# Optimization experiments

Hardware: AMD Instinct MI355X
Metric: run time of the kernel (lower is better)

The kernel has to match this reference:

```python
import jax, jax.numpy as jnp
import numpy as np

LN_EPS = 1e-5
DIM = 128
HEADS = 6
DIM_HEAD = 32
INNER = HEADS * DIM_HEAD          # 192
FF_INNER = int(DIM * 4 * 2 / 3)   # 341 (GEGLU inner dim)
LOCAL_WINDOW = 200
CACHE = 3
COMPRESS = 2
TW = LOCAL_WINDOW + CACHE         # 203
B = 2
T = 12800                         # 32 chunks of 400


def layer_norm(x, w, b):
    m = x.mean(-1, keepdims=True)
    v = ((x - m) ** 2).mean(-1, keepdims=True)
    return (x - m) / jnp.sqrt(v + LN_EPS) * w + b


def apply_rotary(q, k):
    # q, k: (b, h, n, d); standard half-rotation rotary over absolute positions
    d = q.shape[-1]
    n = q.shape[2]
    inv_freq = 1.0 / (10000.0 ** (jnp.arange(0, d, 2, dtype=jnp.float32) / d))
    freqs = jnp.arange(n, dtype=jnp.float32)[:, None] * inv_freq  # (n, d/2)
    emb = jnp.concatenate([freqs, freqs], axis=-1)                # (n, d)
    cos = jnp.cos(emb).astype(q.dtype)
    sin = jnp.sin(emb).astype(q.dtype)

    def rot_half(x):
        x1, x2 = jnp.split(x, 2, axis=-1)
        return jnp.concatenate([-x2, x1], axis=-1)

    rope = lambda x: x * cos + rot_half(x) * sin
    return rope(q), rope(k)


def local_attention(q, k, v, w):
    # causal local attention, look_backward=1 window, look_forward=0 (lucidrains LocalAttention)
    b, h, n, d = q.shape
    nw = n // w
    q, k = apply_rotary(q, k)
    qw = q.reshape(b, h, nw, w, d)

    def look_around(x):
        xw = x.reshape(b, h, nw, w, d)
        prev = jnp.pad(xw[:, :, :-1], ((0, 0), (0, 0), (1, 0), (0, 0), (0, 0)))
        return jnp.concatenate([prev, xw], axis=3)  # (b,h,nw,2w,d)

    kw = look_around(k)
    vw = look_around(v)

    t = jnp.arange(n).reshape(nw, w)
    tk_prev = jnp.pad(t[:-1], ((1, 0), (0, 0)), constant_values=-1)
    tk = jnp.concatenate([tk_prev, t], axis=1)  # (nw, 2w); -1 marks padding
    mask = (t[:, :, None] >= tk[:, None, :]) & (tk[:, None, :] >= 0)  # (nw, w, 2w)

    sim = jnp.einsum('bhwid,bhwjd->bhwij', qw, kw) * (d ** -0.5)
    neg = jnp.finfo(sim.dtype).min
    sim = jnp.where(mask[None, None], sim, neg)
    attn = jax.nn.softmax(sim, axis=-1)
    out = jnp.einsum('bhwij,bhwjd->bhwid', attn, vw)
    return out.reshape(b, h, n, d)


def local_mha(x, ln_w, ln_b, wqkv, wo, window):
    h = layer_norm(x, ln_w, ln_b)
    qkv = h @ wqkv                       # (b, n, 3*INNER)
    q, k, v = jnp.split(qkv, 3, axis=-1)

    def split_heads(t):
        bb, n, _ = t.shape
        return t.reshape(bb, n, HEADS, DIM_HEAD).transpose(0, 2, 1, 3)

    out = local_attention(split_heads(q), split_heads(k), split_heads(v), window)
    bb, hh, n, d = out.shape
    out = out.transpose(0, 2, 1, 3).reshape(bb, n, hh * d)
    return out @ wo


def feed_forward(x, ln_w, ln_b, w1, w2):
    h = layer_norm(x, ln_w, ln_b) @ w1   # (b, n, 2*FF_INNER)
    a, gate = jnp.split(h, 2, axis=-1)
    return (a * jax.nn.gelu(gate, approximate=False)) @ w2


def local_trans(x, ln1_w, ln1_b, wqkv, wo, ln2_w, ln2_b, w1, w2, window):
    n_layers = ln1_w.shape[0]
    for i in range(n_layers):
        x = x + local_mha(x, ln1_w[i], ln1_b[i], wqkv[i], wo[i], window)
        x = x + feed_forward(x, ln2_w[i], ln2_b[i], w1[i], w2[i])
    return x


def setup_inputs() -> dict:
    key = jax.random.key(0)
    ks = jax.random.split(key, 16)
    std = 0.02
    rn = lambda k, shape: jax.random.normal(k, shape, dtype=jnp.float32) * std
    inp = {
        'x': jax.random.normal(ks[0], (B, DIM, T), dtype=jnp.float32),
        'cache_token': jax.random.normal(ks[1], (1, CACHE * COMPRESS, DIM), dtype=jnp.float32),
    }
    ki = 2
    for g in ('dt', 'lt'):
        inp[g + '_ln1_w'] = jnp.ones((2, DIM), jnp.float32)
        inp[g + '_ln1_b'] = jnp.zeros((2, DIM), jnp.float32)
        inp[g + '_wqkv'] = rn(ks[ki], (2, DIM, 3 * INNER)); ki += 1
        inp[g + '_wo'] = rn(ks[ki], (2, INNER, DIM)); ki += 1
        inp[g + '_ln2_w'] = jnp.ones((2, DIM), jnp.float32)
        inp[g + '_ln2_b'] = jnp.zeros((2, DIM), jnp.float32)
        inp[g + '_w1'] = rn(ks[ki], (2, DIM, 2 * FF_INNER)); ki += 1
        inp[g + '_w2'] = rn(ks[ki], (2, FF_INNER, DIM)); ki += 1
    inp['conv_w'] = rn(ks[ki], (DIM, DIM, COMPRESS)); ki += 1
    inp['conv_b'] = jnp.zeros((DIM,), jnp.float32)
    return inp


def reference(x, cache_token,
              dt_ln1_w, dt_ln1_b, dt_wqkv, dt_wo, dt_ln2_w, dt_ln2_b, dt_w1, dt_w2,
              lt_ln1_w, lt_ln1_b, lt_wqkv, lt_wo, lt_ln2_w, lt_ln2_b, lt_w1, lt_w2,
              conv_w, conv_b):
    feat = x.transpose(0, 2, 1)                     # (B, T, C)
    b, t, c = feat.shape
    chunk = LOCAL_WINDOW * COMPRESS                 # 400
    nchunks = t // chunk
    feat = feat.reshape(b, nchunks, chunk, c)
    ct = jnp.broadcast_to(cache_token[:, None], (b, nchunks, CACHE * COMPRESS, c))
    feat = jnp.concatenate([ct, feat], axis=2)      # interleave cache tokens per chunk
    feat = feat.reshape(b, nchunks * (chunk + CACHE * COMPRESS), c)

    # DownTrans: 2-layer local transformer (window 406) + strided conv compress
    feat = local_trans(feat, dt_ln1_w, dt_ln1_b, dt_wqkv, dt_wo,
                       dt_ln2_w, dt_ln2_b, dt_w1, dt_w2, TW * COMPRESS)
    y = jax.lax.conv_general_dilated(
        feat.transpose(0, 2, 1), conv_w, (COMPRESS,), 'VALID',
        dimension_numbers=('NCH', 'OIH', 'NCH')) + conv_b[None, :, None]
    feat = y.transpose(0, 2, 1)                     # (B, n/2, C)

    # remaining depth-2 local transformer (window 203)
    feat = local_trans(feat, lt_ln1_w, lt_ln1_b, lt_wqkv, lt_wo,
                       lt_ln2_w, lt_ln2_b, lt_w1, lt_w2, TW)
    return feat
```

## Files before the change

kernel.cpp:

```cpp
#include <hip/hip_runtime.h>
#include <cstdint>
#include <cstddef>

#define DIM    128
#define HEADS  6
#define INNER  192
#define QKV3   576
#define FFI    341
#define FF2    682
#define GGP    352
#define BATCH  2
#define T_IN   12800
#define N1     12992
#define N2     6496
#define ROWS1  (BATCH * N1)
#define ROWS2  (BATCH * N2)
#define W_DT   406
#define W_LT   203

typedef unsigned short ushortT;
typedef unsigned int u32;
typedef __bf16 bf16x8 __attribute__((ext_vector_type(8)));
typedef float f32x4 __attribute__((ext_vector_type(4)));

__device__ __forceinline__ f32x4 mfma16(bf16x8 a, bf16x8 b, f32x4 c) {
  return __builtin_amdgcn_mfma_f32_16x16x32_bf16(a, b, c, 0, 0, 0);
}
__device__ __forceinline__ ushortT f2bf(float x) {
  union { __bf16 b; ushortT u; } c; c.b = (__bf16)x; return c.u;
}
__device__ __forceinline__ void async_copy16(const ushortT* g, ushortT* l) {
  __builtin_amdgcn_global_load_lds(
      (const __attribute__((address_space(1))) unsigned int*)g,
      (__attribute__((address_space(3))) unsigned int*)l, 16, 0, 0);
}

static constexpr size_t OF_FEAT = 0;
static constexpr size_t OF_H    = OF_FEAT + (size_t)ROWS1 * DIM;
static constexpr size_t OF_QKH  = OF_H + (size_t)ROWS1 * DIM / 2;
static constexpr size_t SZ_QKH  = ((size_t)(ROWS1 + 128) * 384) / 2;
static constexpr size_t OF_AO   = OF_QKH + SZ_QKH;
static constexpr size_t OF_VT   = OF_AO + (size_t)ROWS1 * INNER / 2;
static constexpr size_t SZ_VT   = ((size_t)384 * (N1 + 128)) / 2;
static constexpr size_t OF_GG   = OF_VT + SZ_VT;
static constexpr size_t OF_F2   = OF_GG + (size_t)ROWS1 * GGP / 2;
static constexpr size_t OF_WT   = OF_F2 + (size_t)ROWS2 * DIM;
static constexpr size_t WT_QKV = 0;
static constexpr size_t WT_WO  = 81920;
static constexpr size_t WT_W1  = 106496;
static constexpr size_t WT_W2  = 204800;
static constexpr size_t WT_SET = 249856;
static constexpr size_t OF_CW  = OF_WT + (4 * WT_SET) / 2 + 64;

__global__ void build_feat_kernel(const float* __restrict__ x,
                                  const float* __restrict__ cache,
                                  float* __restrict__ feat) {
  int idx = blockIdx.x * 256 + threadIdx.x;
  if (idx >= ROWS1 * DIM) return;
  int d = idx & 127;
  int row = idx >> 7;
  int b = row / N1;
  int i = row - b * N1;
  int c = i / 406;
  int j = i - c * 406;
  float v;
  if (j < 6) v = cache[j * DIM + d];
  else       v = x[((size_t)b * DIM + d) * T_IN + (c * 400 + j - 6)];
  feat[idx] = v;
}

__global__ __launch_bounds__(256) void ln_kernel(const float* __restrict__ x,
                                                 ushortT* __restrict__ y,
                                                 const float* __restrict__ w,
                                                 const float* __restrict__ bb,
                                                 int rows) {
  int row = blockIdx.x * 4 + (threadIdx.x >> 6);
  if (row >= rows) return;
  int lane = threadIdx.x & 63;
  const float* xr = x + (size_t)row * DIM;
  float2 v = *(const float2*)(xr + lane * 2);
  float s = v.x + v.y;
#pragma unroll
  for (int off = 32; off; off >>= 1) s += __shfl_xor(s, off);
  float mean = s * (1.0f / 128.0f);
  float dx = v.x - mean, dy = v.y - mean;
  float q = dx * dx + dy * dy;
#pragma unroll
  for (int off = 32; off; off >>= 1) q += __shfl_xor(q, off);
  float rstd = rsqrtf(q * (1.0f / 128.0f) + 1e-5f);
  float2 wv = *(const float2*)(w + lane * 2);
  float2 bv = *(const float2*)(bb + lane * 2);
  u32 packed = (u32)f2bf(dx * rstd * wv.x + bv.x) |
               ((u32)f2bf(dy * rstd * wv.y + bv.y) << 16);
  *(u32*)(y + (size_t)row * DIM + lane * 2) = packed;
}

__global__ __launch_bounds__(256) void gemm_nln(
    const ushortT* __restrict__ A, int lda,
    const ushortT* __restrict__ Wt, int ldw,
    const float* __restrict__ C, float* __restrict__ Co,
    int M, int Kpad, int addC,
    const float* __restrict__ lnw, const float* __restrict__ lnb,
    ushortT* __restrict__ hout) {
  __shared__ ushortT As[64 * 32];
  __shared__ ushortT Bs[128 * 32];
  __shared__ float lnS[64][4];
  const int tid = threadIdx.x;
  const int wid = tid >> 6, lane = tid & 63;
  const int ck = lane & 15, quad = lane >> 4;
  const int bm = blockIdx.y * 64;
  const int wr = (wid >> 1) * 32, wc = (wid & 1) * 64;
  const int half = wid & 1;
  f32x4 acc[2][4];
#pragma unroll
  for (int t = 0; t < 2; t++)
#pragma unroll
    for (int u = 0; u < 4; u++) acc[t][u] = (f32x4){0.f, 0.f, 0.f, 0.f};

  for (int k0 = 0; k0 < Kpad; k0 += 32) {
    __syncthreads();
    {
      int idx = wid * 64 + lane;
      int row = idx >> 2, seg = (idx & 3) << 3;
      async_copy16(A + (size_t)(bm + row) * lda + k0 + seg, As + (size_t)(wid * 64) * 8);
    }
#pragma unroll
    for (int c2 = 0; c2 < 2; c2++) {
      int idx = c2 * 256 + wid * 64 + lane;
      int row = idx >> 2, seg = (idx & 3) << 3;
      async_copy16(Wt + (size_t)row * ldw + k0 + seg, Bs + (size_t)(c2 * 256 + wid * 64) * 8);
    }
    __syncthreads();
    bf16x8 af[2], bfr[4];
#pragma unroll
    for (int t = 0; t < 2; t++)
      af[t] = *(const bf16x8*)&As[(wr + t * 16 + ck) * 32 + quad * 8];
#pragma unroll
    for (int u = 0; u < 4; u++)
      bfr[u] = *(const bf16x8*)&Bs[(wc + u * 16 + ck) * 32 + quad * 8];
#pragma unroll
    for (int t = 0; t < 2; t++)
#pragma unroll
      for (int u = 0; u < 4; u++)
        acc[t][u] = mfma16(af[t], bfr[u], acc[t][u]);
  }

  float res[2][4][4];
#pragma unroll
  for (int t = 0; t < 2; t++) {
#pragma unroll
    for (int r = 0; r < 4; r++) {
      int row = bm + wr + t * 16 + quad * 4 + r;
      const float* crow = C + (size_t)row * DIM;
      float* orow = Co + (size_t)row * DIM;
#pragma unroll
      for (int u = 0; u < 4; u++) {
        int col = wc + u * 16 + ck;
        float v = acc[t][u][r];
        if (addC) v += crow[col];
        res[t][r][u] = v;
        orow[col] = v;
      }
    }
  }

  if (hout) {
#pragma unroll
    for (int t = 0; t < 2; t++) {
#pragma unroll
      for (int r = 0; r < 4; r++) {
        float s1 = ((res[t][r][0] + res[t][r][1]) + (res[t][r][2] + res[t][r][3]));
        float s2 = ((res[t][r][0] * res[t][r][0] + res[t][r][1] * res[t][r][1]) +
                    (res[t][r][2] * res[t][r][2] + res[t][r][3] * res[t][r][3]));
        s1 += __shfl_xor(s1, 1); s2 += __shfl_xor(s2, 1);
        s1 += __shfl_xor(s1, 2); s2 += __shfl_xor(s2, 2);
        s1 += __shfl_xor(s1, 4); s2 += __shfl_xor(s2, 4);
        s1 += __shfl_xor(s1, 8); s2 += __shfl_xor(s2, 8);
        if (ck == 0) {
          int rowIn = wr + t * 16 + quad * 4 + r;
          lnS[rowIn][half * 2]     = s1;
          lnS[rowIn][half * 2 + 1] = s2;
        }
      }
    }
    __syncthreads();
    float lw[4], lb[4];
#pragma unroll
    for (int u = 0; u < 4; u++) {
      lw[u] = lnw[wc + u * 16 + ck];
      lb[u] = lnb[wc + u * 16 + ck];
    }
#pragma unroll
    for (int t = 0; t < 2; t++) {
#pragma unroll
      for (int r = 0; r < 4; r++) {
        int rowIn = wr + t * 16 + quad * 4 + r;
        float S1 = lnS[rowIn][0] + lnS[rowIn][2];
        float S2 = lnS[rowIn][1] + lnS[rowIn][3];
        float mean = S1 * (1.0f / 128.0f);
        float var = S2 * (1.0f / 128.0f) - mean * mean;
        float rstd = rsqrtf(var + 1e-5f);
        ushortT* hrow = hout + (size_t)(bm + rowIn) * DIM;
#pragma unroll
        for (int u = 0; u < 4; u++) {
          int col = wc + u * 16 + ck;
          hrow[col] = f2bf((res[t][r][u] - mean) * rstd * lw[u] + lb[u]);
        }
      }
    }
  }
}

__global__ __launch_bounds__(256) void gemm_qkv(
    const ushortT* __restrict__ A,
    const ushortT* __restrict__ Wt,
    ushortT* __restrict__ qkh,
    ushortT* __restrict__ vt,
    int M, int nseq, int nseqP) {
  __shared__ ushortT As[128 * 32];
  __shared__ ushortT Bs[128 * 32];
  const int tid = threadIdx.x;
  const int wid = tid >> 6, lane = tid & 63;
  const int ck = lane & 15, quad = lane >> 4;
  const int bm = blockIdx.y * 128, bn = blockIdx.x * 128;
  const int wr = (wid >> 1) * 64, wc = (wid & 1) * 64;
  f32x4 acc[4][4];
#pragma unroll
  for (int t = 0; t < 4; t++)
#pragma unroll
    for (int u = 0; u < 4; u++) acc[t][u] = (f32x4){0.f, 0.f, 0.f, 0.f};

  for (int k0 = 0; k0 < 128; k0 += 32) {
    __syncthreads();
#pragma unroll
    for (int c2 = 0; c2 < 2; c2++) {
      int idx = c2 * 256 + wid * 64 + lane;
      int row = idx >> 2, seg = (idx & 3) << 3;
      int ar = bm + row; if (ar > M - 1) ar = M - 1;
      async_copy16(A + (size_t)ar * 128 + k0 + seg, As + (size_t)(c2 * 256 + wid * 64) * 8);
      async_copy16(Wt + (size_t)(bn + row) * 128 + k0 + seg, Bs + (size_t)(c2 * 256 + wid * 64) * 8);
    }
    __syncthreads();
    bf16x8 af[4], bfr[4];
#pragma unroll
    for (int t = 0; t < 4; t++)
      af[t] = *(const bf16x8*)&As[(wr + t * 16 + ck) * 32 + quad * 8];
#pragma unroll
    for (int u = 0; u < 4; u++)
      bfr[u] = *(const bf16x8*)&Bs[(wc + u * 16 + ck) * 32 + quad * 8];
#pragma unroll
    for (int t = 0; t < 4; t++)
#pragma unroll
      for (int u = 0; u < 4; u++)
        acc[t][u] = mfma16(af[t], bfr[u], acc[t][u]);
  }

  const int s = bn + wc;
  if (s >= QKV3) return;

  if (s < 384) {
    const bool isQ = s < 192;
    const float SCq = 0.17677669529663687f * 1.4426950408889634f;
    const float invf = 1.0f / powf(10000.0f, (float)ck * (1.0f / 16.0f));
#pragma unroll
    for (int t = 0; t < 4; t++) {
#pragma unroll
      for (int r = 0; r < 4; r++) {
        int row = bm + wr + t * 16 + quad * 4 + r;
        if (row >= M) continue;
        int pos = (row >= nseq) ? row - nseq : row;
        float sn, cs;
        sincosf((float)pos * invf, &sn, &cs);
        ushortT* orow = qkh + (size_t)row * 384;
#pragma unroll
        for (int u = 0; u < 4; u += 2) {
          float a0 = acc[t][u][r], a1 = acc[t][u + 1][r];
          float o0 = a0 * cs - a1 * sn;
          float o1 = a1 * cs + a0 * sn;
          if (isQ) { o0 *= SCq; o1 *= SCq; }
          int c0 = s + u * 16 + ck;
          orow[c0]      = f2bf(o0);
          orow[c0 + 16] = f2bf(o1);
        }
      }
    }
  } else {
#pragma unroll
    for (int t = 0; t < 4; t++) {
      int rowb = bm + wr + t * 16 + quad * 4;
      if (rowb >= M) continue;
      int bb = (rowb >= nseq) ? 1 : 0;
      int posb = rowb - bb * nseq;
#pragma unroll
      for (int u = 0; u < 4; u++) {
        int cv = s - 384 + u * 16 + ck;
        int hh = cv >> 5, d = cv & 31;
        ushort4 o;
        o.x = f2bf(acc[t][u][0]);
        o.y = f2bf(acc[t][u][1]);
        o.z = f2bf(acc[t][u][2]);
        o.w = f2bf(acc[t][u][3]);
        *(ushort4*)(vt + ((size_t)((bb * 6 + hh) * 32 + d)) * nseqP + posb) = o;
      }
    }
  }
}

__global__ __launch_bounds__(256) void gemm_w1g(
    const ushortT* __restrict__ A,
    const ushortT* __restrict__ Wt,
    ushortT* __restrict__ gg,
    int M) {
  __shared__ ushortT As[128 * 32];
  __shared__ ushortT Bs[128 * 32];
  const int tid = threadIdx.x;
  const int wid = tid >> 6, lane = tid & 63;
  const int ck = lane & 15, quad = lane >> 4;
  const int bm = blockIdx.y * 128, bn = blockIdx.x * 128;
  const int wr = (wid >> 1) * 64, wc = (wid & 1) * 64;
  f32x4 acc[4][4];
#pragma unroll
  for (int t = 0; t < 4; t++)
#pragma unroll
    for (int u = 0; u < 4; u++) acc[t][u] = (f32x4){0.f, 0.f, 0.f, 0.f};

  for (int k0 = 0; k0 < 128; k0 += 32) {
    __syncthreads();
#pragma unroll
    for (int c2 = 0; c2 < 2; c2++) {
      int idx = c2 * 256 + wid * 64 + lane;
      int row = idx >> 2, seg = (idx & 3) << 3;
      int ar = bm + row; if (ar > M - 1) ar = M - 1;
      async_copy16(A + (size_t)ar * 128 + k0 + seg, As + (size_t)(c2 * 256 + wid * 64) * 8);
      async_copy16(Wt + (size_t)(bn + row) * 128 + k0 + seg, Bs + (size_t)(c2 * 256 + wid * 64) * 8);
    }
    __syncthreads();
    bf16x8 af[4], bfr[4];
#pragma unroll
    for (int t = 0; t < 4; t++)
      af[t] = *(const bf16x8*)&As[(wr + t * 16 + ck) * 32 + quad * 8];
#pragma unroll
    for (int u = 0; u < 4; u++)
      bfr[u] = *(const bf16x8*)&Bs[(wc + u * 16 + ck) * 32 + quad * 8];
#pragma unroll
    for (int t = 0; t < 4; t++)
#pragma unroll
      for (int u = 0; u < 4; u++)
        acc[t][u] = mfma16(af[t], bfr[u], acc[t][u]);
  }

  const int s = bn + wc;
  if (s >= 704) return;
#pragma unroll
  for (int t = 0; t < 4; t++) {
#pragma unroll
    for (int r = 0; r < 4; r++) {
      int row = bm + wr + t * 16 + quad * 4 + r;
      if (row >= M) continue;
      ushortT* orow = gg + (size_t)row * GGP;
#pragma unroll
      for (int u = 0; u < 4; u += 2) {
        float a  = acc[t][u][r];
        float gt = acc[t][u + 1][r];
        float ge = 0.5f * gt * (1.0f + erff(gt * 0.70710678118654752f));
        int p = ((s + u * 16) >> 5) * 16 + ck;
        orow[p] = f2bf(a * ge);
      }
    }
  }
}

__global__ __launch_bounds__(256) void gemm_f32(
    const float* __restrict__ A, int lda,
    const float* __restrict__ W, int ldw,
    float* __restrict__ C, int ldc,
    int M, int N, int K, int addC, const float* __restrict__ bias) {
  __shared__ float As[16][68];
  __shared__ float Ws[16][68];
  int tid = threadIdx.x;
  int bm = blockIdx.y * 64, bn = blockIdx.x * 64;
  int tx = tid & 15, ty = tid >> 4;
  float acc[4][4] = {{0.f,0.f,0.f,0.f},{0.f,0.f,0.f,0.f},{0.f,0.f,0.f,0.f},{0.f,0.f,0.f,0.f}};
  int arow = tid >> 2;
  int akq = (tid & 3) << 2;
  int wk = tid >> 4;
  int wn = (tid & 15) << 2;
  for (int k0 = 0; k0 < K; k0 += 16) {
    float4 av = *(const float4*)(A + (size_t)(bm + arow) * lda + k0 + akq);
    float4 wv = *(const float4*)(W + (size_t)(k0 + wk) * ldw + bn + wn);
    __syncthreads();
    As[akq + 0][arow] = av.x; As[akq + 1][arow] = av.y;
    As[akq + 2][arow] = av.z; As[akq + 3][arow] = av.w;
    *(float4*)&Ws[wk][wn] = wv;
    __syncthreads();
#pragma unroll
    for (int kk = 0; kk < 16; kk++) {
      float4 a4 = *(const float4*)&As[kk][ty << 2];
      float4 b4 = *(const float4*)&Ws[kk][tx << 2];
      float aa[4] = {a4.x, a4.y, a4.z, a4.w};
      float bv2[4] = {b4.x, b4.y, b4.z, b4.w};
#pragma unroll
      for (int i = 0; i < 4; i++)
#pragma unroll
        for (int j = 0; j < 4; j++)
          acc[i][j] = fmaf(aa[i], bv2[j], acc[i][j]);
    }
  }
#pragma unroll
  for (int i = 0; i < 4; i++) {
    int row = bm + (ty << 2) + i;
    float* crow = C + (size_t)row * ldc;
#pragma unroll
    for (int j = 0; j < 4; j++) {
      int col = bn + (tx << 2) + j;
      float v = acc[i][j];
      if (bias) v += bias[col];
      if (addC) v += crow[col];
      crow[col] = v;
    }
  }
}

__global__ __launch_bounds__(256) void attn_kernel(
    const ushortT* __restrict__ qkh, const ushortT* __restrict__ vt,
    ushortT* __restrict__ out, int nseq, int nseqP, int w, int nw) {
  __shared__ ushortT Ks[128 * 40];
  __shared__ ushortT Vs[32 * 136];
  __shared__ ushortT Ps[4 * 16 * 72];

  const int bx = blockIdx.x;
  const int c = bx % nw;
  const int g = bx / nw;
  const int h = blockIdx.y;
  const int b = blockIdx.z;
  const int tid = threadIdx.x;
  const int wv = tid >> 6;
  const int lane = tid & 63;
  const int ck = lane & 15;
  const int quad = lane >> 4;

  const ushortT* gq = qkh + (size_t)b * nseq * 384;
  const ushortT* gv = vt + ((size_t)(b * 6 + h) * 32) * nseqP;
  const int cw = c * w;
  const int q0 = g * 64;
  const int qt = q0 + wv * 16;
  const bool wave_on = qt < w;

  const int j0 = (c > 0) ? (c - 1) * w : 0;
  const int jend_block = cw + min(q0 + 63, w - 1) + 1;
  const int jend_wave = wave_on ? (cw + min(qt + 15, w - 1) + 1) : 0;

  bf16x8 qf;
  {
    int qrow = cw + min(qt + ck, w - 1);
    qf = *(const bf16x8*)(gq + (size_t)qrow * 384 + h * 32 + quad * 8);
  }

  f32x4 olo = {0.f, 0.f, 0.f, 0.f};
  f32x4 ohi = {0.f, 0.f, 0.f, 0.f};
  float lp[4] = {0.f, 0.f, 0.f, 0.f};
  ushortT* pw = Ps + wv * 16 * 72;

  for (int tb = j0; tb < jend_block; tb += 128) {
    __syncthreads();
    for (int i = tid; i < 512; i += 256) {
      int row = i >> 2, dg = (i & 3) << 3;
      *(float4*)&Ks[row * 40 + dg] =
          *(const float4*)(gq + (size_t)(tb + row) * 384 + 192 + h * 32 + dg);
    }
    for (int i = tid; i < 512; i += 256) {
      int d = i >> 4, kg = (i & 15) << 3;
      *(float4*)&Vs[d * 136 + kg] = *(const float4*)(gv + (size_t)d * nseqP + tb + kg);
    }
    __syncthreads();

    const int glim = min(128, jend_wave - tb);
    for (int g64 = 0; g64 < glim; g64 += 64) {
      int r0 = g64 + 2 * ck;
      bf16x8 kf0 = *(const bf16x8*)&Ks[(r0) * 40 + quad * 8];
      bf16x8 kf1 = *(const bf16x8*)&Ks[(r0 + 1) * 40 + quad * 8];
      bf16x8 kf2 = *(const bf16x8*)&Ks[(r0 + 32) * 40 + quad * 8];
      bf16x8 kf3 = *(const bf16x8*)&Ks[(r0 + 33) * 40 + quad * 8];
      f32x4 z = {0.f, 0.f, 0.f, 0.f};
      f32x4 s0 = mfma16(qf, kf0, z);
      f32x4 s1 = mfma16(qf, kf1, z);
      f32x4 s2 = mfma16(qf, kf2, z);
      f32x4 s3 = mfma16(qf, kf3, z);
      if (tb + g64 + 63 > cw + qt) {
        int key0 = tb + g64 + 2 * ck;
#pragma unroll
        for (int r = 0; r < 4; r++) {
          int qg = cw + qt + quad * 4 + r;
          if (key0 > qg)      s0[r] = -__builtin_inff();
          if (key0 + 1 > qg)  s1[r] = -__builtin_inff();
          if (key0 + 32 > qg) s2[r] = -__builtin_inff();
          if (key0 + 33 > qg) s3[r] = -__builtin_inff();
        }
      }
#pragma unroll
      for (int r = 0; r < 4; r++) {
        float p0 = exp2f(s0[r]);
        float p1 = exp2f(s1[r]);
        float p2 = exp2f(s2[r]);
        float p3 = exp2f(s3[r]);
        lp[r] += (p0 + p1) + (p2 + p3);
        int row72 = (quad * 4 + r) * 72;
        *(u32*)&pw[row72 + 2 * ck]      = (u32)f2bf(p0) | ((u32)f2bf(p1) << 16);
        *(u32*)&pw[row72 + 32 + 2 * ck] = (u32)f2bf(p2) | ((u32)f2bf(p3) << 16);
      }
      bf16x8 pf0 = *(const bf16x8*)&pw[ck * 72 + quad * 8];
      bf16x8 pf1 = *(const bf16x8*)&pw[ck * 72 + 32 + quad * 8];
      bf16x8 vlo0 = *(const bf16x8*)&Vs[ck * 136 + g64 + quad * 8];
      bf16x8 vhi0 = *(const bf16x8*)&Vs[(ck + 16) * 136 + g64 + quad * 8];
      bf16x8 vlo1 = *(const bf16x8*)&Vs[ck * 136 + g64 + 32 + quad * 8];
      bf16x8 vhi1 = *(const bf16x8*)&Vs[(ck + 16) * 136 + g64 + 32 + quad * 8];
      olo = mfma16(pf0, vlo0, olo);
      olo = mfma16(pf1, vlo1, olo);
      ohi = mfma16(pf0, vhi0, ohi);
      ohi = mfma16(pf1, vhi1, ohi);
    }
  }

  if (wave_on) {
#pragma unroll
    for (int r = 0; r < 4; r++) {
      float lr = lp[r];
      lr += __shfl_xor(lr, 1);
      lr += __shfl_xor(lr, 2);
      lr += __shfl_xor(lr, 4);
      lr += __shfl_xor(lr, 8);
      int qi = qt + quad * 4 + r;
      if (qi < w) {
        float inv = 1.0f / lr;
        ushortT* orow = out + ((size_t)b * nseq + cw + qi) * INNER + h * 32;
        orow[ck]      = f2bf(olo[r] * inv);
        orow[ck + 16] = f2bf(ohi[r] * inv);
      }
    }
  }
}

__global__ void wconvert_all_kernel(
    const float* __restrict__ dq, const float* __restrict__ dwo,
    const float* __restrict__ dw1, const float* __restrict__ dw2,
    const float* __restrict__ lq, const float* __restrict__ lwo,
    const float* __restrict__ lw1, const float* __restrict__ lw2,
    const float* __restrict__ convw,
    ushortT* __restrict__ wt, float* __restrict__ cwout) {
  int idx = blockIdx.x * 256 + threadIdx.x;
  const int TOTW = 4 * (int)WT_SET;
  if (idx < TOTW) {
    int s = idx / (int)WT_SET;
    int rem = idx - s * (int)WT_SET;
    int lyr = s & 1;
    const float* Wq = ((s < 2) ? dq : lq) + (size_t)lyr * DIM * QKV3;
    const float* Wo = ((s < 2) ? dwo : lwo) + (size_t)lyr * INNER * DIM;
    const float* W1 = ((s < 2) ? dw1 : lw1) + (size_t)lyr * DIM * FF2;
    const float* W2 = ((s < 2) ? dw2 : lw2) + (size_t)lyr * FFI * DIM;
    float v = 0.f;
    if (rem < (int)WT_WO) {
      int n = rem >> 7, k = rem & 127;
      if (n < QKV3) v = Wq[(size_t)k * QKV3 + n];
    } else if (rem < (int)WT_W1) {
      int r = rem - (int)WT_WO;
      int n = r / INNER, k = r - n * INNER;
      v = Wo[(size_t)k * DIM + n];
    } else if (rem < (int)WT_W2) {
      int r = rem - (int)WT_W1;
      int n = r >> 7, k = r & 127;
      if (n < 704) {
        int blk = n >> 5, wi = n & 31;
        int p = blk * 16 + (wi & 15);
        if (p < FFI) {
          int src = (wi < 16) ? p : FFI + p;
          v = W1[(size_t)k * FF2 + src];
        }
      }
    } else {
      int r = rem - (int)WT_W2;
      int n = r / GGP, k = r - n * GGP;
      if (k < FFI) v = W2[(size_t)k * DIM + n];
    }
    wt[idx] = f2bf(v);
  } else {
    int r = idx - TOTW;
    if (r < 256 * DIM) {
      int kidx = r >> 7, o = r & 127;
      int kk = kidx >> 7, i = kidx & 127;
      cwout[r] = convw[((size_t)o * DIM + i) * 2 + kk];
    }
  }
}

static void run_layer(float* F, float* Fout, ushortT* h, ushortT* qkh, ushortT* vtb,
                      ushortT* attnb, ushortT* ggb, const ushortT* wt,
                      int M, int nseq, int w,
                      const float* ln2w, const float* ln2b,
                      const float* nlnw, const float* nlnb,
                      hipStream_t stream) {
  int nseqP = nseq + 128;
  int gy = (M + 127) / 128;
  int gy64 = M / 64;
  gemm_qkv<<<dim3(5, gy), 256, 0, stream>>>(h, wt + WT_QKV, qkh, vtb, M, nseq, nseqP);
  int nw = nseq / w;
  int qgroups = (w + 63) / 64;
  attn_kernel<<<dim3(nw * qgroups, HEADS, BATCH), 256, 0, stream>>>(qkh, vtb, attnb,
                                                                    nseq, nseqP, w, nw);
  gemm_nln<<<dim3(1, gy64), 256, 0, stream>>>(attnb, INNER, wt + WT_WO, INNER, F, F,
                                              M, INNER, 1, ln2w, ln2b, h);
  gemm_w1g<<<dim3(6, gy), 256, 0, stream>>>(h, wt + WT_W1, ggb, M);
  gemm_nln<<<dim3(1, gy64), 256, 0, stream>>>(ggb, GGP, wt + WT_W2, GGP, F, Fout,
                                              M, GGP, 1, nlnw, nlnb,
                                              nlnw ? h : (ushortT*)nullptr);
}

extern "C" void kernel_launch(void* const* d_in, const int* in_sizes, int n_in,
                              void* d_out, int out_size, void* d_ws, size_t ws_size,
                              hipStream_t stream) {
  const float* x        = (const float*)d_in[0];
  const float* cache    = (const float*)d_in[1];
  const float* dt_ln1_w = (const float*)d_in[2];
  const float* dt_ln1_b = (const float*)d_in[3];
  const float* dt_wqkv  = (const float*)d_in[4];
  const float* dt_wo    = (const float*)d_in[5];
  const float* dt_ln2_w = (const float*)d_in[6];
  const float* dt_ln2_b = (const float*)d_in[7];
  const float* dt_w1    = (const float*)d_in[8];
  const float* dt_w2    = (const float*)d_in[9];
  const float* lt_ln1_w = (const float*)d_in[10];
  const float* lt_ln1_b = (const float*)d_in[11];
  const float* lt_wqkv  = (const float*)d_in[12];
  const float* lt_wo    = (const float*)d_in[13];
  const float* lt_ln2_w = (const float*)d_in[14];
  const float* lt_ln2_b = (const float*)d_in[15];
  const float* lt_w1    = (const float*)d_in[16];
  const float* lt_w2    = (const float*)d_in[17];
  const float* conv_w   = (const float*)d_in[18];
  const float* conv_b   = (const float*)d_in[19];

  float* ws     = (float*)d_ws;
  float* feat   = ws + OF_FEAT;
  ushortT* h    = (ushortT*)(ws + OF_H);
  ushortT* qkh  = (ushortT*)(ws + OF_QKH);
  ushortT* attnb= (ushortT*)(ws + OF_AO);
  ushortT* vtb  = (ushortT*)(ws + OF_VT);
  ushortT* ggb  = (ushortT*)(ws + OF_GG);
  float* feat2  = ws + OF_F2;
  ushortT* wt   = (ushortT*)(ws + OF_WT);
  float* cw     = ws + OF_CW;
  float* outf   = (float*)d_out;

  {
    int total = 4 * (int)WT_SET + 256 * DIM;
    wconvert_all_kernel<<<(total + 255) / 256, 256, 0, stream>>>(
        dt_wqkv, dt_wo, dt_w1, dt_w2, lt_wqkv, lt_wo, lt_w1, lt_w2,
        conv_w, wt, cw);
  }

  build_feat_kernel<<<(ROWS1 * DIM + 255) / 256, 256, 0, stream>>>(x, cache, feat);
  ln_kernel<<<ROWS1 / 4, 256, 0, stream>>>(feat, h, dt_ln1_w, dt_ln1_b, ROWS1);

  run_layer(feat, feat, h, qkh, vtb, attnb, ggb, wt + 0 * WT_SET,
            ROWS1, N1, W_DT,
            dt_ln2_w, dt_ln2_b, dt_ln1_w + DIM, dt_ln1_b + DIM, stream);
  run_layer(feat, feat, h, qkh, vtb, attnb, ggb, wt + 1 * WT_SET,
            ROWS1, N1, W_DT,
            dt_ln2_w + DIM, dt_ln2_b + DIM, nullptr, nullptr, stream);

  gemm_f32<<<dim3(DIM / 64, ROWS2 / 64), 256, 0, stream>>>(feat, 256, cw, DIM, feat2, DIM,
                                                           ROWS2, DIM, 256, 0, conv_b);
  ln_kernel<<<ROWS2 / 4, 256, 0, stream>>>(feat2, h, lt_ln1_w, lt_ln1_b, ROWS2);

  run_layer(feat2, feat2, h, qkh, vtb, attnb, ggb, wt + 2 * WT_SET,
            ROWS2, N2, W_LT,
            lt_ln2_w, lt_ln2_b, lt_ln1_w + DIM, lt_ln1_b + DIM, stream);
  run_layer(feat2, outf, h, qkh, vtb, attnb, ggb, wt + 3 * WT_SET,
            ROWS2, N2, W_LT,
            lt_ln2_w + DIM, lt_ln2_b + DIM, nullptr, nullptr, stream);
}
```

Baseline: 576.5 us.

## Fuse conv compress into bf16 MFMA GEMM with LN epilogue, precompute rope table

The strided conv used to run as a separate fp32 SIMT GEMM followed by a LayerNorm kernel. It now reuses the bf16 MFMA gemm_nln kernel. The last DownTrans layer's W2 GEMM writes bf16 output directly, which is then read as the conv input, and the conv GEMM applies bias plus the next LayerNorm in its epilogue. Rotary sin/cos values are also precomputed once into a table, replacing per-row sincosf in the QKV epilogue. This removes a slow fp32 kernel, an LN pass and an fp32 feature write, at the cost of bf16 rounding on the conv input and weights.

```diff
diff --git a/kernel.cpp b/kernel.cpp
--- a/kernel.cpp
+++ b/kernel.cpp
@@ -51,6 +51,8 @@
 static constexpr size_t WT_W2  = 204800;
 static constexpr size_t WT_SET = 249856;
 static constexpr size_t OF_CW  = OF_WT + (4 * WT_SET) / 2 + 64;
+static constexpr size_t OF_ROPE = OF_CW + (128 * 256) / 2 + 64;
+static constexpr size_t OF_H2  = OF_ROPE + (size_t)N1 * 32;
 
 __global__ void build_feat_kernel(const float* __restrict__ x,
                                   const float* __restrict__ cache,
@@ -99,9 +101,10 @@
     const ushortT* __restrict__ A, int lda,
     const ushortT* __restrict__ Wt, int ldw,
     const float* __restrict__ C, float* __restrict__ Co,
+    const float* __restrict__ bias,
     int M, int Kpad, int addC,
     const float* __restrict__ lnw, const float* __restrict__ lnb,
-    ushortT* __restrict__ hout) {
+    ushortT* __restrict__ hout, ushortT* __restrict__ bfout) {
   __shared__ ushortT As[64 * 32];
   __shared__ ushortT Bs[128 * 32];
   __shared__ float lnS[64][4];
@@ -145,6 +148,11 @@
         acc[t][u] = mfma16(af[t], bfr[u], acc[t][u]);
   }
 
+  float bv4[4] = {0.f, 0.f, 0.f, 0.f};
+  if (bias) {
+#pragma unroll
+    for (int u = 0; u < 4; u++) bv4[u] = bias[wc + u * 16 + ck];
+  }
   float res[2][4][4];
 #pragma unroll
   for (int t = 0; t < 2; t++) {
@@ -152,14 +160,22 @@
     for (int r = 0; r < 4; r++) {
       int row = bm + wr + t * 16 + quad * 4 + r;
       const float* crow = C + (size_t)row * DIM;
-      float* orow = Co + (size_t)row * DIM;
 #pragma unroll
       for (int u = 0; u < 4; u++) {
         int col = wc + u * 16 + ck;
-        float v = acc[t][u][r];
+        float v = acc[t][u][r] + bv4[u];
         if (addC) v += crow[col];
         res[t][r][u] = v;
-        orow[col] = v;
+      }
+      if (Co) {
+        float* orow = Co + (size_t)row * DIM;
+#pragma unroll
+        for (int u = 0; u < 4; u++) orow[wc + u * 16 + ck] = res[t][r][u];
+      }
+      if (bfout) {
+        ushortT* brow = bfout + (size_t)row * DIM;
+#pragma unroll
+        for (int u = 0; u < 4; u++) brow[wc + u * 16 + ck] = f2bf(res[t][r][u]);
       }
     }
   }
@@ -214,6 +230,7 @@
 __global__ __launch_bounds__(256) void gemm_qkv(
     const ushortT* __restrict__ A,
     const ushortT* __restrict__ Wt,
+    const float2* __restrict__ rope,
     ushortT* __restrict__ qkh,
     ushortT* __restrict__ vt,
     int M, int nseq, int nseqP) {
@@ -261,7 +278,6 @@
   if (s < 384) {
     const bool isQ = s < 192;
     const float SCq = 0.17677669529663687f * 1.4426950408889634f;
-    const float invf = 1.0f / powf(10000.0f, (float)ck * (1.0f / 16.0f));
 #pragma unroll
     for (int t = 0; t < 4; t++) {
 #pragma unroll
@@ -269,8 +285,8 @@
         int row = bm + wr + t * 16 + quad * 4 + r;
         if (row >= M) continue;
         int pos = (row >= nseq) ? row - nseq : row;
-        float sn, cs;
-        sincosf((float)pos * invf, &sn, &cs);
+        float2 cssn = rope[pos * 16 + ck];
+        float cs = cssn.x, sn = cssn.y;
         ushortT* orow = qkh + (size_t)row * 384;
 #pragma unroll
         for (int u = 0; u < 4; u += 2) {
@@ -366,57 +382,6 @@
         int p = ((s + u * 16) >> 5) * 16 + ck;
         orow[p] = f2bf(a * ge);
       }
-    }
-  }
-}
-
-__global__ __launch_bounds__(256) void gemm_f32(
-    const float* __restrict__ A, int lda,
-    const float* __restrict__ W, int ldw,
-    float* __restrict__ C, int ldc,
-    int M, int N, int K, int addC, const float* __restrict__ bias) {
-  __shared__ float As[16][68];
-  __shared__ float Ws[16][68];
-  int tid = threadIdx.x;
-  int bm = blockIdx.y * 64, bn = blockIdx.x * 64;
-  int tx = tid & 15, ty = tid >> 4;
-  float acc[4][4] = {{0.f,0.f,0.f,0.f},{0.f,0.f,0.f,0.f},{0.f,0.f,0.f,0.f},{0.f,0.f,0.f,0.f}};
-  int arow = tid >> 2;
-  int akq = (tid & 3) << 2;
-  int wk = tid >> 4;
-  int wn = (tid & 15) << 2;
-  for (int k0 = 0; k0 < K; k0 += 16) {
-    float4 av = *(const float4*)(A + (size_t)(bm + arow) * lda + k0 + akq);
-    float4 wv = *(const float4*)(W + (size_t)(k0 + wk) * ldw + bn + wn);
-    __syncthreads();
-    As[akq + 0][arow] = av.x; As[akq + 1][arow] = av.y;
-    As[akq + 2][arow] = av.z; As[akq + 3][arow] = av.w;
-    *(float4*)&Ws[wk][wn] = wv;
-    __syncthreads();
-#pragma unroll
-    for (int kk = 0; kk < 16; kk++) {
-      float4 a4 = *(const float4*)&As[kk][ty << 2];
-      float4 b4 = *(const float4*)&Ws[kk][tx << 2];
-      float aa[4] = {a4.x, a4.y, a4.z, a4.w};
-      float bv2[4] = {b4.x, b4.y, b4.z, b4.w};
-#pragma unroll
-      for (int i = 0; i < 4; i++)
-#pragma unroll
-        for (int j = 0; j < 4; j++)
-          acc[i][j] = fmaf(aa[i], bv2[j], acc[i][j]);
-    }
-  }
-#pragma unroll
-  for (int i = 0; i < 4; i++) {
-    int row = bm + (ty << 2) + i;
-    float* crow = C + (size_t)row * ldc;
-#pragma unroll
-    for (int j = 0; j < 4; j++) {
-      int col = bn + (tx << 2) + j;
-      float v = acc[i][j];
-      if (bias) v += bias[col];
-      if (addC) v += crow[col];
-      crow[col] = v;
     }
   }
 }
@@ -546,9 +511,11 @@
     const float* __restrict__ lq, const float* __restrict__ lwo,
     const float* __restrict__ lw1, const float* __restrict__ lw2,
     const float* __restrict__ convw,
-    ushortT* __restrict__ wt, float* __restrict__ cwout) {
+    ushortT* __restrict__ wt, ushortT* __restrict__ cwt,
+    float2* __restrict__ rope) {
   int idx = blockIdx.x * 256 + threadIdx.x;
   const int TOTW = 4 * (int)WT_SET;
+  const int CWN = 128 * 256;
   if (idx < TOTW) {
     int s = idx / (int)WT_SET;
     int rem = idx - s * (int)WT_SET;
@@ -582,36 +549,45 @@
       if (k < FFI) v = W2[(size_t)k * DIM + n];
     }
     wt[idx] = f2bf(v);
+  } else if (idx < TOTW + CWN) {
+    int r = idx - TOTW;
+    int o = r >> 8, k = r & 255;
+    int kk = k >> 7, i = k & 127;
+    cwt[r] = f2bf(convw[((size_t)o * DIM + i) * 2 + kk]);
   } else {
-    int r = idx - TOTW;
-    if (r < 256 * DIM) {
-      int kidx = r >> 7, o = r & 127;
-      int kk = kidx >> 7, i = kidx & 127;
-      cwout[r] = convw[((size_t)o * DIM + i) * 2 + kk];
-    }
-  }
-}
-
-static void run_layer(float* F, float* Fout, ushortT* h, ushortT* qkh, ushortT* vtb,
+    int r = idx - TOTW - CWN;
+    if (r < N1 * 16) {
+      int pos = r >> 4, k = r & 15;
+      float invf = 1.0f / powf(10000.0f, (float)k * (1.0f / 16.0f));
+      float sn, cs;
+      sincosf((float)pos * invf, &sn, &cs);
+      rope[r] = make_float2(cs, sn);
+    }
+  }
+}
+
+static void run_layer(float* F, float* Fout, ushortT* hbuf, ushortT* qkh, ushortT* vtb,
                       ushortT* attnb, ushortT* ggb, const ushortT* wt,
+                      const float2* rope,
                       int M, int nseq, int w,
                       const float* ln2w, const float* ln2b,
                       const float* nlnw, const float* nlnb,
-                      hipStream_t stream) {
+                      ushortT* w2bf, hipStream_t stream) {
   int nseqP = nseq + 128;
   int gy = (M + 127) / 128;
   int gy64 = M / 64;
-  gemm_qkv<<<dim3(5, gy), 256, 0, stream>>>(h, wt + WT_QKV, qkh, vtb, M, nseq, nseqP);
+  gemm_qkv<<<dim3(5, gy), 256, 0, stream>>>(hbuf, wt + WT_QKV, rope, qkh, vtb, M, nseq, nseqP);
   int nw = nseq / w;
   int qgroups = (w + 63) / 64;
   attn_kernel<<<dim3(nw * qgroups, HEADS, BATCH), 256, 0, stream>>>(qkh, vtb, attnb,
                                                                     nseq, nseqP, w, nw);
   gemm_nln<<<dim3(1, gy64), 256, 0, stream>>>(attnb, INNER, wt + WT_WO, INNER, F, F,
-                                              M, INNER, 1, ln2w, ln2b, h);
-  gemm_w1g<<<dim3(6, gy), 256, 0, stream>>>(h, wt + WT_W1, ggb, M);
+                                              nullptr, M, INNER, 1, ln2w, ln2b,
+                                              hbuf, nullptr);
+  gemm_w1g<<<dim3(6, gy), 256, 0, stream>>>(hbuf, wt + WT_W1, ggb, M);
   gemm_nln<<<dim3(1, gy64), 256, 0, stream>>>(ggb, GGP, wt + WT_W2, GGP, F, Fout,
-                                              M, GGP, 1, nlnw, nlnb,
-                                              nlnw ? h : (ushortT*)nullptr);
+                                              nullptr, M, GGP, 1, nlnw, nlnb,
+                                              nlnw ? hbuf : (ushortT*)nullptr, w2bf);
 }
 
 extern "C" void kernel_launch(void* const* d_in, const int* in_sizes, int n_in,
@@ -647,34 +623,37 @@
   ushortT* ggb  = (ushortT*)(ws + OF_GG);
   float* feat2  = ws + OF_F2;
   ushortT* wt   = (ushortT*)(ws + OF_WT);
-  float* cw     = ws + OF_CW;
+  ushortT* cwt  = (ushortT*)(ws + OF_CW);
+  float2* rope  = (float2*)(ws + OF_ROPE);
+  ushortT* h2   = (ushortT*)(ws + OF_H2);
   float* outf   = (float*)d_out;
 
   {
-    int total = 4 * (int)WT_SET + 256 * DIM;
+    int total = 4 * (int)WT_SET + 128 * 256 + N1 * 16;
     wconvert_all_kernel<<<(total + 255) / 256, 256, 0, stream>>>(
         dt_wqkv, dt_wo, dt_w1, dt_w2, lt_wqkv, lt_wo, lt_w1, lt_w2,
-        conv_w, wt, cw);
+        conv_w, wt, cwt, rope);
   }
 
   build_feat_kernel<<<(ROWS1 * DIM + 255) / 256, 256, 0, stream>>>(x, cache, feat);
   ln_kernel<<<ROWS1 / 4, 256, 0, stream>>>(feat, h, dt_ln1_w, dt_ln1_b, ROWS1);
 
-  run_layer(feat, feat, h, qkh, vtb, attnb, ggb, wt + 0 * WT_SET,
+  run_layer(feat, feat, h, qkh, vtb, attnb, ggb, wt + 0 * WT_SET, rope,
             ROWS1, N1, W_DT,
-            dt_ln2_w, dt_ln2_b, dt_ln1_w + DIM, dt_ln1_b + DIM, stream);
-  run_layer(feat, feat, h, qkh, vtb, attnb, ggb, wt + 1 * WT_SET,
+            dt_ln2_w, dt_ln2_b, dt_ln1_w + DIM, dt_ln1_b + DIM, nullptr, stream);
+  run_layer(feat, nullptr, h, qkh, vtb, attnb, ggb, wt + 1 * WT_SET, rope,
             ROWS1, N1, W_DT,
-            dt_ln2_w + DIM, dt_ln2_b + DIM, nullptr, nullptr, stream);
-
-  gemm_f32<<<dim3(DIM / 64, ROWS2 / 64), 256, 0, stream>>>(feat, 256, cw, DIM, feat2, DIM,
-                                                           ROWS2, DIM, 256, 0, conv_b);
-  ln_kernel<<<ROWS2 / 4, 256, 0, stream>>>(feat2, h, lt_ln1_w, lt_ln1_b, ROWS2);
-
-  run_layer(feat2, feat2, h, qkh, vtb, attnb, ggb, wt + 2 * WT_SET,
+            dt_ln2_w + DIM, dt_ln2_b + DIM, nullptr, nullptr, h, stream);
+
+  gemm_nln<<<dim3(1, ROWS2 / 64), 256, 0, stream>>>(h, 256, cwt, 256,
+                                                    feat2, feat2, conv_b,
+                                                    ROWS2, 256, 0,
+                                                    lt_ln1_w, lt_ln1_b, h2, nullptr);
+
+  run_layer(feat2, feat2, h2, qkh, vtb, attnb, ggb, wt + 2 * WT_SET, rope,
             ROWS2, N2, W_LT,
-            lt_ln2_w, lt_ln2_b, lt_ln1_w + DIM, lt_ln1_b + DIM, stream);
-  run_layer(feat2, outf, h, qkh, vtb, attnb, ggb, wt + 3 * WT_SET,
+            lt_ln2_w, lt_ln2_b, lt_ln1_w + DIM, lt_ln1_b + DIM, nullptr, stream);
+  run_layer(feat2, outf, h2, qkh, vtb, attnb, ggb, wt + 3 * WT_SET, rope,
             ROWS2, N2, W_LT,
-            lt_ln2_w + DIM, lt_ln2_b + DIM, nullptr, nullptr, stream);
-}
+            lt_ln2_w + DIM, lt_ln2_b + DIM, nullptr, nullptr, nullptr, stream);
+}
```

Result: no change. 573.2 us (-0.6%).
